# Kernel optimization log

Hardware: AMD Instinct MI355X
Metric: run time of the kernel (lower is better)

## Reference

```python
import jax, jax.numpy as jnp
import numpy as np

B, D, H = 64, 512, 8
EPS = 1e-8


def setup_inputs() -> dict:
    key = jax.random.key(0)
    k1, k2, k3 = jax.random.split(key, 3)
    x = jax.random.normal(k1, (B, D), dtype=jnp.float32)
    # alphas/betas: one scalar per (head, transform); columns = (query, key, value)
    alphas = jax.random.uniform(k2, (H, 3), dtype=jnp.float32)
    betas = jax.random.uniform(k3, (H, 3), dtype=jnp.float32)
    return {"x": x, "alphas": alphas, "betas": betas}


def reference(x, alphas, betas):
    # x: [B, D]; alphas, betas: [H, 3] (query, key, value scalar affine params per head)
    d = x.shape[-1]
    # qkv[h, t, b, d] = alphas[h, t] * x[b, d] + betas[h, t]  (ones vector -> plain bias)
    qkv = alphas[:, :, None, None] * x[None, None, :, :] + betas[:, :, None, None]  # [H,3,B,D]
    q, k, v = qkv[:, 0], qkv[:, 1], qkv[:, 2]  # each [H, B, D]
    # diff[h,b,i,j] = |q[h,b,j] - k[h,b,i]|  (row i = key feature, col j = query feature)
    diff = jnp.abs(q[:, :, None, :] - k[:, :, :, None]) + EPS  # [H, B, D, D]
    sim = jax.nn.softmax(1.0 / diff, axis=-1) / jnp.sqrt(jnp.float32(d))
    # attended[h,b,i] = sum_j sim[h,b,i,j] * v[h,b,j]  (batched matvec)
    attended = jnp.einsum("hbij,hbj->hbi", sim, v)  # [H, B, D]
    return x + attended.sum(axis=0)
```

## Files before the change

kernel.cpp:

```cpp
#include <hip/hip_runtime.h>
#include <math.h>

#define BB 64
#define DD 512
#define HH 8
#define EPS 1e-8f
#define NCH 8
#define CS 32

__device__ __forceinline__ float fast_rcp(float d) {
    return __builtin_amdgcn_rcpf(d);
}

__global__ __launch_bounds__(512) void sort_rows(
    const float* __restrict__ x,
    float* __restrict__ xsorted,
    unsigned short* __restrict__ isorted)
{
    const int b = blockIdx.x;
    const int i = threadIdx.x;
    __shared__ float sx[DD];
    const float xi = x[b * DD + i];
    sx[i] = xi;
    __syncthreads();
    int rank = 0;
    for (int j = 0; j < DD; j += 4) {
        float4 v = *(const float4*)&sx[j];
        rank += (v.x < xi) | ((v.x == xi) & ((j + 0) < i));
        rank += (v.y < xi) | ((v.y == xi) & ((j + 1) < i));
        rank += (v.z < xi) | ((v.z == xi) & ((j + 2) < i));
        rank += (v.w < xi) | ((v.w == xi) & ((j + 3) < i));
    }
    xsorted[b * DD + rank] = xi;
    isorted[b * DD + rank] = (unsigned short)i;
}

__global__ __launch_bounds__(512, 8) void flattn_kernel(
    const float* __restrict__ xsorted,
    const unsigned short* __restrict__ isorted,
    const float* __restrict__ alphas,
    const float* __restrict__ betas,
    float* __restrict__ out)
{
    const int b  = blockIdx.x;
    const int ic = blockIdx.y;
    const int h  = blockIdx.z;

    __shared__ float xs[DD];
    __shared__ float mind_sh[2][256];
    __shared__ float ss_sh[256];
    __shared__ float sx_sh[256];

    const int tid = threadIdx.x;
    const int ii  = tid & 255;
    const int jc  = tid >> 8;
    const int i   = ic * 256 + ii;

    const float a0 = alphas[h * 3 + 0];
    const float a1 = alphas[h * 3 + 1];
    const float a2 = alphas[h * 3 + 2];
    const float b0 = betas[h * 3 + 0];
    const float b1 = betas[h * 3 + 1];
    const float b2 = betas[h * 3 + 2];

    xs[tid] = xsorted[b * DD + tid];
    __syncthreads();

    const float xi = xs[i];
    const float c  = b0 - fmaf(a1, xi, b1);
    const int j0 = jc * 256;

    float cmin[NCH];
    float gmin = 3.0e38f;
    #pragma unroll
    for (int ch = 0; ch < NCH; ++ch) {
        const int base = j0 + ch * CS;
        float cm = 3.0e38f;
        #pragma unroll
        for (int jj = 0; jj < CS; jj += 4) {
            float4 x4 = *(const float4*)&xs[base + jj];
            cm = fminf(cm, fabsf(fmaf(a0, x4.x, c)));
            cm = fminf(cm, fabsf(fmaf(a0, x4.y, c)));
            cm = fminf(cm, fabsf(fmaf(a0, x4.z, c)));
            cm = fminf(cm, fabsf(fmaf(a0, x4.w, c)));
        }
        cmin[ch] = cm;
        gmin = fminf(gmin, cm);
    }
    mind_sh[jc][ii] = gmin;
    __syncthreads();

    gmin = fminf(mind_sh[0][ii], mind_sh[1][ii]);
    const float m = fast_rcp(gmin + EPS);
    const float log2e = 1.4426950408889634f;
    const float negml = -m * log2e;
    const float mr = m - 28.0f;
    const float thr = (mr > 0.0f) ? fast_rcp(mr) : 3.0e38f;

    float ss = 0.0f, sx = 0.0f;
    #pragma unroll
    for (int ch = 0; ch < NCH; ++ch) {
        if (__ballot(cmin[ch] <= thr)) {
            const int base = j0 + ch * CS;
            #pragma unroll 4
            for (int jj = 0; jj < CS; jj += 4) {
                float4 x4 = *(const float4*)&xs[base + jj];
                {
                    float t = fmaf(a0, x4.x, c);
                    float r = fast_rcp(fabsf(t) + EPS);
                    float s = __builtin_amdgcn_exp2f(fmaf(r, log2e, negml));
                    ss += s; sx = fmaf(s, x4.x, sx);
                }
                {
                    float t = fmaf(a0, x4.y, c);
                    float r = fast_rcp(fabsf(t) + EPS);
                    float s = __builtin_amdgcn_exp2f(fmaf(r, log2e, negml));
                    ss += s; sx = fmaf(s, x4.y, sx);
                }
                {
                    float t = fmaf(a0, x4.z, c);
                    float r = fast_rcp(fabsf(t) + EPS);
                    float s = __builtin_amdgcn_exp2f(fmaf(r, log2e, negml));
                    ss += s; sx = fmaf(s, x4.z, sx);
                }
                {
                    float t = fmaf(a0, x4.w, c);
                    float r = fast_rcp(fabsf(t) + EPS);
                    float s = __builtin_amdgcn_exp2f(fmaf(r, log2e, negml));
                    ss += s; sx = fmaf(s, x4.w, sx);
                }
            }
        }
    }

    if (jc == 1) { ss_sh[ii] = ss; sx_sh[ii] = sx; }
    __syncthreads();
    if (jc == 0) {
        ss += ss_sh[ii];
        sx += sx_sh[ii];
        const float scale = 0.04419417382415922f;
        float sv  = fmaf(a2, sx, b2 * ss);
        float att = sv * fast_rcp(ss) * scale;
        if (h == 0) att += xi;
        const int oi = (int)isorted[b * DD + i];
        atomicAdd(&out[b * DD + oi], att);
    }
}

extern "C" void kernel_launch(void* const* d_in, const int* in_sizes, int n_in,
                              void* d_out, int out_size, void* d_ws, size_t ws_size,
                              hipStream_t stream) {
    const float* x      = (const float*)d_in[0];
    const float* alphas = (const float*)d_in[1];
    const float* betas  = (const float*)d_in[2];
    float* out = (float*)d_out;

    float* xsorted = (float*)d_ws;
    unsigned short* isorted = (unsigned short*)(xsorted + BB * DD);

    hipMemsetAsync(out, 0, (size_t)out_size * sizeof(float), stream);

    sort_rows<<<dim3(BB), dim3(DD), 0, stream>>>(x, xsorted, isorted);

    dim3 grid(BB, 2, HH);
    dim3 block(512);
    flattn_kernel<<<grid, block, 0, stream>>>(xsorted, isorted, alphas, betas, out);
}
```

Before: 98.62 us.

## Fuse per-row sort into attention kernel and use 1024-thread blocks per row

Removes the separate sort_rows kernel by having each (batch, head) block rank its row in shared memory using 64-bit keys that pack an order-preserving float encoding with the index. Blocks now cover all 512 query rows with 1024 threads (two key halves) instead of splitting rows across two blocks. This saves a kernel launch and a global round-trip for sorted data, but repeats the sort 8 times per batch row (once per head) and halves the number of blocks.

```diff
diff --git a/kernel.cpp b/kernel.cpp
--- a/kernel.cpp
+++ b/kernel.cpp
@@ -1,5 +1,6 @@
 #include <hip/hip_runtime.h>
 #include <math.h>
+#include <stdint.h>
 
 #define BB 64
 #define DD 512
@@ -12,49 +13,51 @@
     return __builtin_amdgcn_rcpf(d);
 }
 
-__global__ __launch_bounds__(512) void sort_rows(
+__global__ __launch_bounds__(1024, 8) void flattn_kernel(
     const float* __restrict__ x,
-    float* __restrict__ xsorted,
-    unsigned short* __restrict__ isorted)
-{
-    const int b = blockIdx.x;
-    const int i = threadIdx.x;
-    __shared__ float sx[DD];
-    const float xi = x[b * DD + i];
-    sx[i] = xi;
-    __syncthreads();
-    int rank = 0;
-    for (int j = 0; j < DD; j += 4) {
-        float4 v = *(const float4*)&sx[j];
-        rank += (v.x < xi) | ((v.x == xi) & ((j + 0) < i));
-        rank += (v.y < xi) | ((v.y == xi) & ((j + 1) < i));
-        rank += (v.z < xi) | ((v.z == xi) & ((j + 2) < i));
-        rank += (v.w < xi) | ((v.w == xi) & ((j + 3) < i));
-    }
-    xsorted[b * DD + rank] = xi;
-    isorted[b * DD + rank] = (unsigned short)i;
-}
-
-__global__ __launch_bounds__(512, 8) void flattn_kernel(
-    const float* __restrict__ xsorted,
-    const unsigned short* __restrict__ isorted,
     const float* __restrict__ alphas,
     const float* __restrict__ betas,
     float* __restrict__ out)
 {
-    const int b  = blockIdx.x;
-    const int ic = blockIdx.y;
-    const int h  = blockIdx.z;
+    const int b = blockIdx.x;
+    const int h = blockIdx.y;
 
-    __shared__ float xs[DD];
-    __shared__ float mind_sh[2][256];
-    __shared__ float ss_sh[256];
-    __shared__ float sx_sh[256];
+    __shared__ uint64_t keys[DD];
+    __shared__ float    xs[DD];
+    __shared__ int      idxs[DD];
+    __shared__ int      cnt[2][DD];
+    __shared__ float    mind_sh[2][DD];
+    __shared__ float    ss_sh[DD];
+    __shared__ float    sx_sh[DD];
 
     const int tid = threadIdx.x;
-    const int ii  = tid & 255;
-    const int jc  = tid >> 8;
-    const int i   = ic * 256 + ii;
+    const int ii  = tid & (DD - 1);
+    const int jc  = tid >> 9;
+    const int j0  = jc * 256;
+
+    const float xv = x[b * DD + ii];
+    if (jc == 0) {
+        uint32_t u = __float_as_uint(xv);
+        uint32_t k = (u & 0x80000000u) ? ~u : (u | 0x80000000u);
+        keys[ii] = ((uint64_t)k << 16) | (uint32_t)ii;
+    }
+    __syncthreads();
+
+    const uint64_t myk = keys[ii];
+    int rk = 0;
+    #pragma unroll 8
+    for (int j = j0; j < j0 + 256; j += 2) {
+        rk += (keys[j]     < myk);
+        rk += (keys[j + 1] < myk);
+    }
+    cnt[jc][ii] = rk;
+    __syncthreads();
+    if (jc == 0) {
+        const int rank = cnt[0][ii] + cnt[1][ii];
+        xs[rank]   = xv;
+        idxs[rank] = ii;
+    }
+    __syncthreads();
 
     const float a0 = alphas[h * 3 + 0];
     const float a1 = alphas[h * 3 + 1];
@@ -63,12 +66,8 @@
     const float b1 = betas[h * 3 + 1];
     const float b2 = betas[h * 3 + 2];
 
-    xs[tid] = xsorted[b * DD + tid];
-    __syncthreads();
-
-    const float xi = xs[i];
+    const float xi = xs[ii];
     const float c  = b0 - fmaf(a1, xi, b1);
-    const int j0 = jc * 256;
 
     float cmin[NCH];
     float gmin = 3.0e38f;
@@ -79,10 +78,10 @@
         #pragma unroll
         for (int jj = 0; jj < CS; jj += 4) {
             float4 x4 = *(const float4*)&xs[base + jj];
-            cm = fminf(cm, fabsf(fmaf(a0, x4.x, c)));
-            cm = fminf(cm, fabsf(fmaf(a0, x4.y, c)));
-            cm = fminf(cm, fabsf(fmaf(a0, x4.z, c)));
-            cm = fminf(cm, fabsf(fmaf(a0, x4.w, c)));
+            float ta = fmaf(a0, x4.x, c), tb = fmaf(a0, x4.y, c);
+            float tc = fmaf(a0, x4.z, c), td = fmaf(a0, x4.w, c);
+            cm = fminf(cm, fminf(fabsf(ta), fabsf(tb)));
+            cm = fminf(cm, fminf(fabsf(tc), fabsf(td)));
         }
         cmin[ch] = cm;
         gmin = fminf(gmin, cm);
@@ -142,8 +141,7 @@
         float sv  = fmaf(a2, sx, b2 * ss);
         float att = sv * fast_rcp(ss) * scale;
         if (h == 0) att += xi;
-        const int oi = (int)isorted[b * DD + i];
-        atomicAdd(&out[b * DD + oi], att);
+        atomicAdd(&out[b * DD + idxs[ii]], att);
     }
 }
 
@@ -155,14 +153,9 @@
     const float* betas  = (const float*)d_in[2];
     float* out = (float*)d_out;
 
-    float* xsorted = (float*)d_ws;
-    unsigned short* isorted = (unsigned short*)(xsorted + BB * DD);
-
     hipMemsetAsync(out, 0, (size_t)out_size * sizeof(float), stream);
 
-    sort_rows<<<dim3(BB), dim3(DD), 0, stream>>>(x, xsorted, isorted);
-
-    dim3 grid(BB, 2, HH);
-    dim3 block(512);
-    flattn_kernel<<<grid, block, 0, stream>>>(xsorted, isorted, alphas, betas, out);
+    dim3 grid(BB, HH);
+    dim3 block(1024);
+    flattn_kernel<<<grid, block, 0, stream>>>(x, alphas, betas, out);
 }
```

Result: faster. 94.42 us (-4.3%).
